# Performance work log

Hardware: AMD Instinct MI355X
Metric: run time of the kernel (lower is better)

The kernel has to match this reference:

```python
import jax, jax.numpy as jnp
import numpy as np

B, L, E = 4, 2048, 1024
H, HS = 16, 64  # head_num, head_size; E == H*HS


def setup_inputs() -> dict:
    key = jax.random.key(0)
    k1, k2, k3 = jax.random.split(key, 3)
    x = jax.random.normal(k1, (B, L, E), dtype=jnp.float32)
    W_attn = jax.random.normal(k2, (E, 3 * H * HS), dtype=jnp.float32) * (E ** -0.5)
    W_ffn = jax.random.normal(k3, (H * HS, E), dtype=jnp.float32) * ((H * HS) ** -0.5)
    return {"x": x, "W_attn": W_attn, "W_ffn": W_ffn}


def reference(x, W_attn, W_ffn):
    b, l, _ = x.shape
    z = x @ W_attn  # [B, L, 3*H*HS]
    # NOTE: original splits as (k, q, v) in that order
    k, q, v = jnp.split(z, 3, axis=2)
    k = k.reshape(b, l, H, HS).transpose(0, 2, 1, 3)  # [B,H,L,HS]
    q = q.reshape(b, l, H, HS).transpose(0, 2, 1, 3)
    v = v.reshape(b, l, H, HS).transpose(0, 2, 1, 3)
    # scores[i, j] = k_i . q_j (k plays the row role, q the column role)
    scores = jnp.einsum('bhid,bhjd->bhij', k, q) / (HS ** 0.5)
    idx = jnp.arange(l)
    causal = idx[None, :] > idx[:, None]  # True where j > i (masked out)
    scores = jnp.where(causal[None, None], -jnp.inf, scores)
    attn = jax.nn.softmax(scores, axis=-1)  # softmax over j (the q index)
    y = jnp.einsum('bhij,bhjd->bhid', attn, v)  # [B,H,L,HS]
    y = y.transpose(0, 2, 1, 3).reshape(b, l, H * HS)
    return y @ W_ffn
```

## Files before the change

### kernel.cpp

```cpp
#include <hip/hip_runtime.h>
#include <hip/hip_bf16.h>

typedef __attribute__((ext_vector_type(8))) short bf16x8;
typedef __attribute__((ext_vector_type(4))) float f32x4;
typedef __attribute__((ext_vector_type(2))) float f32x2;

__device__ __forceinline__ short f2b(float f) {
    unsigned u = __builtin_bit_cast(unsigned, f);
    unsigned r = (u + 0x7FFFu + ((u >> 16) & 1u)) >> 16;
    return (short)r;
}

__device__ __forceinline__ unsigned cvt_pk_bf16(float lo, float hi) {
    unsigned r;
    asm("v_cvt_pk_bf16_f32 %0, %1, %2" : "=v"(r) : "v"(lo), "v"(hi));
    return r;
}

__device__ __forceinline__ float fexp2(float x) {
    float r;
    asm("v_exp_f32 %0, %1" : "=v"(r) : "v"(x));
    return r;
}

__device__ __forceinline__ f32x2 pk_add(f32x2 a, f32x2 b) {
    f32x2 d;
    asm("v_pk_add_f32 %0, %1, %2" : "=v"(d) : "v"(a), "v"(b));
    return d;
}

__device__ __forceinline__ void gload_lds16(const void* g, void* l) {
    __builtin_amdgcn_global_load_lds((const __attribute__((address_space(1))) unsigned*)g,
                                     (__attribute__((address_space(3))) unsigned*)l, 16, 0, 0);
}

__global__ void conv_swz(const float* __restrict__ in, short* __restrict__ out, long nch) {
    long i = (long)blockIdx.x * blockDim.x + threadIdx.x;
    long stride = (long)gridDim.x * blockDim.x;
    for (; i < nch; i += stride) {
        long m = i >> 7;
        int ch = (int)(i & 127);
        int p = (ch & ~7) | ((ch ^ (int)m) & 7);
        const float4* s = (const float4*)(in + i * 8);
        float4 a = s[0], b = s[1];
        bf16x8 ov;
        ov[0] = f2b(a.x); ov[1] = f2b(a.y); ov[2] = f2b(a.z); ov[3] = f2b(a.w);
        ov[4] = f2b(b.x); ov[5] = f2b(b.y); ov[6] = f2b(b.z); ov[7] = f2b(b.w);
        *(bf16x8*)(out + (m << 10) + p * 8) = ov;
    }
}

__global__ void transpose_swz(const float* __restrict__ in, short* __restrict__ outT, int R, int C) {
    __shared__ float t[32][33];
    int c0 = blockIdx.x * 32, r0 = blockIdx.y * 32;
    int tx = threadIdx.x, ty = threadIdx.y;
    #pragma unroll
    for (int j = 0; j < 4; ++j)
        t[ty + j * 8][tx] = in[(long)(r0 + ty + j * 8) * C + c0 + tx];
    __syncthreads();
    #pragma unroll
    for (int j = 0; j < 4; ++j) {
        int n = c0 + ty + j * 8;
        int k = r0 + tx;
        int kp = (k & ~63) | ((((k >> 3) ^ n) & 7) << 3) | (k & 7);
        outT[(long)n * R + kp] = f2b(t[tx][ty + j * 8]);
    }
}

__global__ void vtrans_swz(const short* __restrict__ vrow, short* __restrict__ vT) {
    __shared__ short t[64][66];
    const int bh = blockIdx.x & 63;
    const int li0 = ((blockIdx.x >> 6) & 31) << 6;
    const int tid = threadIdx.x;
    const short* src = vrow + ((long)bh * 2048 + li0) * 64;
    {
        int id0 = tid, id1 = tid + 256;
        int r0 = id0 >> 3, c0 = id0 & 7;
        int r1 = id1 >> 3, c1 = id1 & 7;
        *(bf16x8*)&t[r0][c0 * 8] = *(const bf16x8*)&src[r0 * 64 + c0 * 8];
        *(bf16x8*)&t[r1][c1 * 8] = *(const bf16x8*)&src[r1 * 64 + c1 * 8];
    }
    __syncthreads();
    const int d = tid >> 2, part = tid & 3;
    short* dst = vT + ((long)bh * 64 + d) * 2048 + li0;
    const int sw = d & 7;
    #pragma unroll
    for (int cc = 0; cc < 2; ++cc) {
        int cl = part * 2 + cc;
        bf16x8 val;
        #pragma unroll
        for (int i = 0; i < 8; ++i) val[i] = t[cl * 8 + i][d];
        *(bf16x8*)&dst[(cl ^ sw) * 8] = val;
    }
}

template<int MODE>
__launch_bounds__(256, 4)
__global__ void gemm_nt(const short* __restrict__ A, const short* __restrict__ Bt,
                        int M, int N, int K,
                        short* __restrict__ qrole, short* __restrict__ krole,
                        short* __restrict__ vT, float* __restrict__ out) {
    __shared__ __align__(16) short As[128][64];
    __shared__ __align__(16) short Bs[128][64];
    const int tid = threadIdx.x;
    const int lane = tid & 63;
    const int wid = tid >> 6;
    const int wm = wid >> 1, wn = wid & 1;
    const int m0 = blockIdx.y * 128, n0 = blockIdx.x * 128;
    const int r16 = lane & 15, g = lane >> 4;
    const int sw = r16 & 7;
    const char* Ab = (const char*)A;
    const char* Bb = (const char*)Bt;
    const long Kb = (long)K * 2;
    f32x4 acc[4][4] = {};
    for (int k0 = 0; k0 < K; k0 += 64) {
        #pragma unroll
        for (int it = 0; it < 4; ++it) {
            int id = it * 256 + tid;
            int r = id >> 3, cch = id & 7;
            gload_lds16(Ab + (long)(m0 + r) * Kb + k0 * 2 + cch * 16, (char*)As + id * 16);
            gload_lds16(Bb + (long)(n0 + r) * Kb + k0 * 2 + cch * 16, (char*)Bs + id * 16);
        }
        __syncthreads();
        #pragma unroll
        for (int kk = 0; kk < 2; ++kk) {
            bf16x8 af[4], bfr[4];
            #pragma unroll
            for (int m = 0; m < 4; ++m)
                af[m] = *(const bf16x8*)&As[wm * 64 + m * 16 + r16][((kk * 4 + g) ^ sw) * 8];
            #pragma unroll
            for (int n = 0; n < 4; ++n)
                bfr[n] = *(const bf16x8*)&Bs[wn * 64 + n * 16 + r16][((kk * 4 + g) ^ sw) * 8];
            #pragma unroll
            for (int m = 0; m < 4; ++m)
                #pragma unroll
                for (int n = 0; n < 4; ++n)
                    acc[m][n] = __builtin_amdgcn_mfma_f32_16x16x32_bf16(af[m], bfr[n], acc[m][n], 0, 0, 0);
        }
        __syncthreads();
    }
    #pragma unroll
    for (int m = 0; m < 4; ++m) {
        #pragma unroll
        for (int n = 0; n < 4; ++n) {
            #pragma unroll
            for (int r = 0; r < 4; ++r) {
                int row = m0 + wm * 64 + m * 16 + g * 4 + r;
                int col = n0 + wn * 64 + n * 16 + r16;
                float v = acc[m][n][r];
                if (MODE != 1) {
                    int which = col >> 10, cc = col & 1023;
                    int h = cc >> 6, d = cc & 63;
                    int b = row >> 11, li = row & 2047;
                    int bh = b * 16 + h;
                    if (which == 0)      qrole[((long)bh * 2048 + li) * 64 + d] = f2b(v * 0.18033688f);
                    else if (which == 1) krole[((long)bh * 2048 + li) * 64 + (d ^ ((li & 7) << 3))] = f2b(v);
                    else if (MODE == 2)  vT[((long)bh * 2048 + li) * 64 + d] = f2b(v);
                    else                 vT[((long)bh * 64 + d) * 2048 + ((li & ~63) | ((li & 63) ^ ((d & 7) << 3)))] = f2b(v);
                } else {
                    out[(long)row * N + col] = v;
                }
            }
        }
    }
}

__launch_bounds__(256, 3)
__global__ void attn_kernel(const short* __restrict__ qrole, const short* __restrict__ krole,
                            const short* __restrict__ vT, short* __restrict__ y) {
    __shared__ __align__(16) short K_lds[2][64][64];
    __shared__ __align__(16) short V_lds[2][64][64];
    __shared__ __align__(16) short P_lds[4][16][64];
    const int tid = threadIdx.x, lane = tid & 63, w = tid >> 6;
    const int r16 = lane & 15, g = lane >> 4;
    const int idb = blockIdx.x;
    const int bh = idb & 63;
    const int c = 15 - ((idb >> 6) & 15);
    const int q0 = c << 7;
    const int T = 2 * c + 2;
    const short* qb = qrole + (long)bh * (2048 * 64);
    const char* kbyte = (const char*)(krole + (long)bh * (2048 * 64));
    const char* vbyte = (const char*)(vT + (long)bh * (64 * 2048));
    const int b = bh >> 4, h = bh & 15;

    bf16x8 qf[2][2];
    #pragma unroll
    for (int m = 0; m < 2; ++m)
        #pragma unroll
        for (int ks = 0; ks < 2; ++ks)
            qf[m][ks] = *(const bf16x8*)&qb[(long)(q0 + m * 64 + w * 16 + r16) * 64 + ks * 32 + g * 8];

    f32x4 o[2][4] = {};
    float mr[2], lr[2];
    #pragma unroll
    for (int m = 0; m < 2; ++m) { mr[m] = -1e30f; lr[m] = 0.f; }

    const int rr = tid >> 3, cch = tid & 7;
    const char* kg0 = kbyte + rr * 128 + cch * 16;
    const char* kg1 = kbyte + (32 + rr) * 128 + cch * 16;
    const char* vg0 = vbyte + rr * 4096 + cch * 16;
    const char* vg1 = vbyte + (32 + rr) * 4096 + cch * 16;
    char* Kb_ = (char*)&K_lds[0][0][0];
    char* Vb_ = (char*)&V_lds[0][0][0];
    const int ld0 = tid * 16, ld1 = (256 + tid) * 16;

    gload_lds16(kg0, Kb_ + ld0);
    gload_lds16(kg1, Kb_ + ld1);
    gload_lds16(vg0, Vb_ + ld0);
    gload_lds16(vg1, Vb_ + ld1);

    const int psw = (r16 & 7) << 4;
    char* prow = (char*)&P_lds[w][r16][0];

    for (int t = 0; t < T; ++t) {
        __syncthreads();
        const int cur = t & 1;
        if (t + 1 < T) {
            long adv = (long)(t + 1) * 8192;
            long advv = (long)(t + 1) * 128;
            char* kdst = Kb_ + (cur ^ 1) * 8192;
            char* vdst = Vb_ + (cur ^ 1) * 8192;
            gload_lds16(kg0 + adv, kdst + ld0);
            gload_lds16(kg1 + adv, kdst + ld1);
            gload_lds16(vg0 + advv, vdst + ld0);
            gload_lds16(vg1 + advv, vdst + ld1);
        }
        const int jt = t << 6;
        const char* kbase = Kb_ + cur * 8192;
        const char* vbase = Vb_ + cur * 8192;

        bf16x8 kfr[2][4], vfr[2][4];
        #pragma unroll
        for (int ks = 0; ks < 2; ++ks)
            #pragma unroll
            for (int n = 0; n < 4; ++n) {
                const int off = ((ks * 64 + g * 16) ^ psw);
                kfr[ks][n] = *(const bf16x8*)(kbase + (n * 16 + r16) * 128 + off);
                vfr[ks][n] = *(const bf16x8*)(vbase + (n * 16 + r16) * 128 + off);
            }

        #pragma unroll
        for (int m = 0; m < 2; ++m) {
            const int qbase = q0 + m * 64 + w * 16;
            if (jt > qbase + 15) continue;

            f32x4 s[4] = {};
            __builtin_amdgcn_s_setprio(1);
            #pragma unroll
            for (int ks = 0; ks < 2; ++ks)
                #pragma unroll
                for (int n = 0; n < 4; ++n)
                    s[n] = __builtin_amdgcn_mfma_f32_16x16x32_bf16(kfr[ks][n], qf[m][ks], s[n], 0, 0, 0);
            __builtin_amdgcn_s_setprio(0);
            if (jt + 63 > qbase) {
                const int i = qbase + r16;
                #pragma unroll
                for (int n = 0; n < 4; ++n)
                    #pragma unroll
                    for (int r = 0; r < 4; ++r)
                        if (jt + n * 16 + g * 4 + r > i) s[n][r] = -1e30f;
            }
            float a0 = fmaxf(fmaxf(s[0][0], s[0][1]), s[0][2]);
            float a1 = fmaxf(fmaxf(s[0][3], s[1][0]), s[1][1]);
            float a2 = fmaxf(fmaxf(s[1][2], s[1][3]), s[2][0]);
            float a3 = fmaxf(fmaxf(s[2][1], s[2][2]), s[2][3]);
            float a4 = fmaxf(fmaxf(s[3][0], s[3][1]), s[3][2]);
            float b0 = fmaxf(fmaxf(a0, a1), a2);
            float b1 = fmaxf(fmaxf(a3, a4), s[3][3]);
            float tm = fmaxf(b0, b1);
            tm = fmaxf(tm, __shfl_xor(tm, 16));
            tm = fmaxf(tm, __shfl_xor(tm, 32));
            if (__any(tm > mr[m] + 11.5f)) {
                float mn = fmaxf(mr[m], tm);
                float sc = fexp2(mr[m] - mn);
                mr[m] = mn;
                lr[m] *= sc;
                float scr[4];
                #pragma unroll
                for (int r = 0; r < 4; ++r) scr[r] = __shfl(sc, (g << 2) + r);
                #pragma unroll
                for (int nd = 0; nd < 4; ++nd)
                    #pragma unroll
                    for (int r = 0; r < 4; ++r)
                        o[m][nd][r] *= scr[r];
            }
            const float nm = -mr[m];
            f32x2 nm2; nm2.x = nm; nm2.y = nm;
            float p[4][4];
            #pragma unroll
            for (int n = 0; n < 4; ++n) {
                f32x2 lo; lo.x = s[n][0]; lo.y = s[n][1];
                f32x2 hi; hi.x = s[n][2]; hi.y = s[n][3];
                f32x2 e01 = pk_add(lo, nm2);
                f32x2 e23 = pk_add(hi, nm2);
                p[n][0] = fexp2(e01.x);
                p[n][1] = fexp2(e01.y);
                p[n][2] = fexp2(e23.x);
                p[n][3] = fexp2(e23.y);
                unsigned w0 = cvt_pk_bf16(p[n][0], p[n][1]);
                unsigned w1 = cvt_pk_bf16(p[n][2], p[n][3]);
                unsigned long long dw = ((unsigned long long)w1 << 32) | w0;
                *(unsigned long long*)(prow + ((n * 32 + g * 8) ^ psw)) = dw;
            }
            float l0 = (p[0][0] + p[0][1]) + (p[0][2] + p[0][3]);
            float l1 = (p[1][0] + p[1][1]) + (p[1][2] + p[1][3]);
            float l2 = (p[2][0] + p[2][1]) + (p[2][2] + p[2][3]);
            float l3 = (p[3][0] + p[3][1]) + (p[3][2] + p[3][3]);
            float lsum = (l0 + l1) + (l2 + l3);
            lsum += __shfl_xor(lsum, 16);
            lsum += __shfl_xor(lsum, 32);
            lr[m] += lsum;
            __builtin_amdgcn_s_setprio(1);
            #pragma unroll
            for (int ks = 0; ks < 2; ++ks) {
                bf16x8 pf = *(const bf16x8*)(prow + ((ks * 64 + g * 16) ^ psw));
                #pragma unroll
                for (int nd = 0; nd < 4; ++nd)
                    o[m][nd] = __builtin_amdgcn_mfma_f32_16x16x32_bf16(pf, vfr[ks][nd], o[m][nd], 0, 0, 0);
            }
            __builtin_amdgcn_s_setprio(0);
        }
    }
    #pragma unroll
    for (int m = 0; m < 2; ++m) {
        float inv[4];
        #pragma unroll
        for (int r = 0; r < 4; ++r) inv[r] = 1.0f / __shfl(lr[m], (g << 2) + r);
        const int li0 = q0 + m * 64 + w * 16 + (g << 2);
        #pragma unroll
        for (int nd = 0; nd < 4; ++nd)
            #pragma unroll
            for (int r = 0; r < 4; ++r) {
                int li = li0 + r;
                int sub = ((nd * 2 + (r16 >> 3)) ^ li) & 7;
                int kp = h * 64 + sub * 8 + (r16 & 7);
                y[(long)(b * 2048 + li) * 1024 + kp] = f2b(o[m][nd][r] * inv[r]);
            }
    }
}

extern "C" void kernel_launch(void* const* d_in, const int* in_sizes, int n_in,
                              void* d_out, int out_size, void* d_ws, size_t ws_size,
                              hipStream_t stream) {
    const float* x  = (const float*)d_in[0];
    const float* Wa = (const float*)d_in[1];
    const float* Wf = (const float*)d_in[2];
    float* out = (float*)d_out;
    char* ws = (char*)d_ws;
    short* xb  = (short*)(ws);
    short* wab = (short*)(ws + (16l << 20));
    short* wfb = (short*)(ws + (22l << 20));
    short* qr  = (short*)(ws + (24l << 20));
    short* kr  = (short*)(ws + (40l << 20));
    short* vt  = (short*)(ws + (56l << 20));
    short* vrow = (short*)(ws + (72l << 20));

    conv_swz<<<2048, 256, 0, stream>>>(x, xb, (long)8192 * 128);
    transpose_swz<<<dim3(96, 32), dim3(32, 8), 0, stream>>>(Wa, wab, 1024, 3072);
    transpose_swz<<<dim3(32, 32), dim3(32, 8), 0, stream>>>(Wf, wfb, 1024, 1024);
    if (ws_size >= (89ull << 20)) {
        gemm_nt<2><<<dim3(24, 64), 256, 0, stream>>>(xb, wab, 8192, 3072, 1024, qr, kr, vrow, nullptr);
        vtrans_swz<<<2048, 256, 0, stream>>>(vrow, vt);
    } else {
        gemm_nt<0><<<dim3(24, 64), 256, 0, stream>>>(xb, wab, 8192, 3072, 1024, qr, kr, vt, nullptr);
    }
    attn_kernel<<<1024, 256, 0, stream>>>(qr, kr, vt, xb);
    gemm_nt<1><<<dim3(8, 64), 256, 0, stream>>>(xb, wfb, 8192, 1024, 1024, nullptr, nullptr, nullptr, out);
}
```

Before: 171.7 us.

## Widen attention KV tile to 128 keys per iteration

The attention loop now processes 128 keys per step instead of 64. This halves the number of iterations and barriers, and widens the K/V double buffers and the P scratch to match. K and V fragments are now read from LDS inside the MFMA loops instead of being preloaded into registers. The occupancy hint drops from 3 to 2 blocks because LDS use is larger. In exchange, the diagonal tile does extra masked work for the first row group, and fewer blocks are resident to hide latency.

After: 168.7 us. No clear change (-1.7%).

```diff
diff --git a/kernel.cpp b/kernel.cpp
--- a/kernel.cpp
+++ b/kernel.cpp
@@ -165,19 +165,19 @@
     }
 }
 
-__launch_bounds__(256, 3)
+__launch_bounds__(256, 2)
 __global__ void attn_kernel(const short* __restrict__ qrole, const short* __restrict__ krole,
                             const short* __restrict__ vT, short* __restrict__ y) {
-    __shared__ __align__(16) short K_lds[2][64][64];
-    __shared__ __align__(16) short V_lds[2][64][64];
-    __shared__ __align__(16) short P_lds[4][16][64];
+    __shared__ __align__(16) short K_lds[2][128][64];
+    __shared__ __align__(16) short V_lds[2][64][128];
+    __shared__ __align__(16) short P_lds[4][16][128];
     const int tid = threadIdx.x, lane = tid & 63, w = tid >> 6;
     const int r16 = lane & 15, g = lane >> 4;
     const int idb = blockIdx.x;
     const int bh = idb & 63;
     const int c = 15 - ((idb >> 6) & 15);
     const int q0 = c << 7;
-    const int T = 2 * c + 2;
+    const int T = c + 1;
     const short* qb = qrole + (long)bh * (2048 * 64);
     const char* kbyte = (const char*)(krole + (long)bh * (2048 * 64));
     const char* vbyte = (const char*)(vT + (long)bh * (64 * 2048));
@@ -195,19 +195,16 @@
     #pragma unroll
     for (int m = 0; m < 2; ++m) { mr[m] = -1e30f; lr[m] = 0.f; }
 
-    const int rr = tid >> 3, cch = tid & 7;
-    const char* kg0 = kbyte + rr * 128 + cch * 16;
-    const char* kg1 = kbyte + (32 + rr) * 128 + cch * 16;
-    const char* vg0 = vbyte + rr * 4096 + cch * 16;
-    const char* vg1 = vbyte + (32 + rr) * 4096 + cch * 16;
+    const char* kgp = kbyte + (long)tid * 16;
+    const char* vgp = vbyte + (tid >> 4) * 4096 + (tid & 15) * 16;
     char* Kb_ = (char*)&K_lds[0][0][0];
     char* Vb_ = (char*)&V_lds[0][0][0];
-    const int ld0 = tid * 16, ld1 = (256 + tid) * 16;
-
-    gload_lds16(kg0, Kb_ + ld0);
-    gload_lds16(kg1, Kb_ + ld1);
-    gload_lds16(vg0, Vb_ + ld0);
-    gload_lds16(vg1, Vb_ + ld1);
+
+    #pragma unroll
+    for (int it = 0; it < 4; ++it) {
+        gload_lds16(kgp + it * 4096, Kb_ + tid * 16 + it * 4096);
+        gload_lds16(vgp + (long)it * 65536, Vb_ + tid * 16 + it * 4096);
+    }
 
     const int psw = (r16 & 7) << 4;
     char* prow = (char*)&P_lds[w][r16][0];
@@ -216,58 +213,50 @@
         __syncthreads();
         const int cur = t & 1;
         if (t + 1 < T) {
-            long adv = (long)(t + 1) * 8192;
-            long advv = (long)(t + 1) * 128;
-            char* kdst = Kb_ + (cur ^ 1) * 8192;
-            char* vdst = Vb_ + (cur ^ 1) * 8192;
-            gload_lds16(kg0 + adv, kdst + ld0);
-            gload_lds16(kg1 + adv, kdst + ld1);
-            gload_lds16(vg0 + advv, vdst + ld0);
-            gload_lds16(vg1 + advv, vdst + ld1);
-        }
-        const int jt = t << 6;
-        const char* kbase = Kb_ + cur * 8192;
-        const char* vbase = Vb_ + cur * 8192;
-
-        bf16x8 kfr[2][4], vfr[2][4];
-        #pragma unroll
-        for (int ks = 0; ks < 2; ++ks)
-            #pragma unroll
-            for (int n = 0; n < 4; ++n) {
-                const int off = ((ks * 64 + g * 16) ^ psw);
-                kfr[ks][n] = *(const bf16x8*)(kbase + (n * 16 + r16) * 128 + off);
-                vfr[ks][n] = *(const bf16x8*)(vbase + (n * 16 + r16) * 128 + off);
-            }
+            const char* ksrc = kgp + (long)(t + 1) * 16384;
+            const char* vsrc = vgp + (long)(t + 1) * 256;
+            char* kdst = Kb_ + (cur ^ 1) * 16384;
+            char* vdst = Vb_ + (cur ^ 1) * 16384;
+            #pragma unroll
+            for (int it = 0; it < 4; ++it) {
+                gload_lds16(ksrc + it * 4096, kdst + tid * 16 + it * 4096);
+                gload_lds16(vsrc + (long)it * 65536, vdst + tid * 16 + it * 4096);
+            }
+        }
+        const int jt = t << 7;
+        const char* kbase = Kb_ + cur * 16384;
+        const char* vbase = Vb_ + cur * 16384;
+        const bool diag = (t == T - 1);
 
         #pragma unroll
         for (int m = 0; m < 2; ++m) {
             const int qbase = q0 + m * 64 + w * 16;
-            if (jt > qbase + 15) continue;
-
-            f32x4 s[4] = {};
+
+            f32x4 s[8] = {};
             __builtin_amdgcn_s_setprio(1);
             #pragma unroll
             for (int ks = 0; ks < 2; ++ks)
                 #pragma unroll
-                for (int n = 0; n < 4; ++n)
-                    s[n] = __builtin_amdgcn_mfma_f32_16x16x32_bf16(kfr[ks][n], qf[m][ks], s[n], 0, 0, 0);
+                for (int n = 0; n < 8; ++n) {
+                    bf16x8 kf = *(const bf16x8*)(kbase + (n * 16 + r16) * 128 + ((ks * 64 + g * 16) ^ psw));
+                    s[n] = __builtin_amdgcn_mfma_f32_16x16x32_bf16(kf, qf[m][ks], s[n], 0, 0, 0);
+                }
             __builtin_amdgcn_s_setprio(0);
-            if (jt + 63 > qbase) {
+            if (diag) {
                 const int i = qbase + r16;
                 #pragma unroll
-                for (int n = 0; n < 4; ++n)
+                for (int n = 0; n < 8; ++n)
                     #pragma unroll
                     for (int r = 0; r < 4; ++r)
                         if (jt + n * 16 + g * 4 + r > i) s[n][r] = -1e30f;
             }
-            float a0 = fmaxf(fmaxf(s[0][0], s[0][1]), s[0][2]);
-            float a1 = fmaxf(fmaxf(s[0][3], s[1][0]), s[1][1]);
-            float a2 = fmaxf(fmaxf(s[1][2], s[1][3]), s[2][0]);
-            float a3 = fmaxf(fmaxf(s[2][1], s[2][2]), s[2][3]);
-            float a4 = fmaxf(fmaxf(s[3][0], s[3][1]), s[3][2]);
-            float b0 = fmaxf(fmaxf(a0, a1), a2);
-            float b1 = fmaxf(fmaxf(a3, a4), s[3][3]);
-            float tm = fmaxf(b0, b1);
+            float tn[8];
+            #pragma unroll
+            for (int n = 0; n < 8; ++n)
+                tn[n] = fmaxf(fmaxf(s[n][0], s[n][1]), fmaxf(s[n][2], s[n][3]));
+            float u0 = fmaxf(fmaxf(tn[0], tn[1]), fmaxf(tn[2], tn[3]));
+            float u1 = fmaxf(fmaxf(tn[4], tn[5]), fmaxf(tn[6], tn[7]));
+            float tm = fmaxf(u0, u1);
             tm = fmaxf(tm, __shfl_xor(tm, 16));
             tm = fmaxf(tm, __shfl_xor(tm, 32));
             if (__any(tm > mr[m] + 11.5f)) {
@@ -286,37 +275,35 @@
             }
             const float nm = -mr[m];
             f32x2 nm2; nm2.x = nm; nm2.y = nm;
-            float p[4][4];
-            #pragma unroll
-            for (int n = 0; n < 4; ++n) {
+            float lsum = 0.f;
+            #pragma unroll
+            for (int n = 0; n < 8; ++n) {
                 f32x2 lo; lo.x = s[n][0]; lo.y = s[n][1];
                 f32x2 hi; hi.x = s[n][2]; hi.y = s[n][3];
                 f32x2 e01 = pk_add(lo, nm2);
                 f32x2 e23 = pk_add(hi, nm2);
-                p[n][0] = fexp2(e01.x);
-                p[n][1] = fexp2(e01.y);
-                p[n][2] = fexp2(e23.x);
-                p[n][3] = fexp2(e23.y);
-                unsigned w0 = cvt_pk_bf16(p[n][0], p[n][1]);
-                unsigned w1 = cvt_pk_bf16(p[n][2], p[n][3]);
+                float p0 = fexp2(e01.x);
+                float p1 = fexp2(e01.y);
+                float p2 = fexp2(e23.x);
+                float p3 = fexp2(e23.y);
+                unsigned w0 = cvt_pk_bf16(p0, p1);
+                unsigned w1 = cvt_pk_bf16(p2, p3);
                 unsigned long long dw = ((unsigned long long)w1 << 32) | w0;
                 *(unsigned long long*)(prow + ((n * 32 + g * 8) ^ psw)) = dw;
-            }
-            float l0 = (p[0][0] + p[0][1]) + (p[0][2] + p[0][3]);
-            float l1 = (p[1][0] + p[1][1]) + (p[1][2] + p[1][3]);
-            float l2 = (p[2][0] + p[2][1]) + (p[2][2] + p[2][3]);
-            float l3 = (p[3][0] + p[3][1]) + (p[3][2] + p[3][3]);
-            float lsum = (l0 + l1) + (l2 + l3);
+                lsum += (p0 + p1) + (p2 + p3);
+            }
             lsum += __shfl_xor(lsum, 16);
             lsum += __shfl_xor(lsum, 32);
             lr[m] += lsum;
             __builtin_amdgcn_s_setprio(1);
             #pragma unroll
-            for (int ks = 0; ks < 2; ++ks) {
+            for (int ks = 0; ks < 4; ++ks) {
                 bf16x8 pf = *(const bf16x8*)(prow + ((ks * 64 + g * 16) ^ psw));
                 #pragma unroll
-                for (int nd = 0; nd < 4; ++nd)
-                    o[m][nd] = __builtin_amdgcn_mfma_f32_16x16x32_bf16(pf, vfr[ks][nd], o[m][nd], 0, 0, 0);
+                for (int nd = 0; nd < 4; ++nd) {
+                    bf16x8 vf = *(const bf16x8*)(vbase + (nd * 16 + r16) * 256 + ((ks * 64 + g * 16) ^ psw));
+                    o[m][nd] = __builtin_amdgcn_mfma_f32_16x16x32_bf16(pf, vf, o[m][nd], 0, 0, 0);
+                }
             }
             __builtin_amdgcn_s_setprio(0);
         }
```
